# Performance work log

Hardware: AMD Instinct MI355X
Metric: run time of the kernel (lower is better)

## Reference

```python
import jax, jax.numpy as jnp
import numpy as np

N = 200_000        # atoms
E = 800_000        # directed edges (pairs e, e^1 are mutual reverses)
H = 512            # hidden_size
AF = 133           # atom_feat_size
BF = 14            # bond_feat_size
B = 4096           # num graphs


def setup_inputs() -> dict:
    key = jax.random.key(0)
    ks = jax.random.split(key, 8)
    atom_hiddens = jax.random.normal(ks[0], (N, H), dtype=jnp.float32)
    # undirected bonds, then interleave as (src,dst),(dst,src) so rev[e] = e ^ 1
    src = jax.random.randint(ks[1], (E // 2,), 0, N, dtype=jnp.int32)
    dst = jax.random.randint(ks[2], (E // 2,), 0, N, dtype=jnp.int32)
    heads = jnp.stack([src, dst], axis=1).reshape(-1)   # [E]
    tails = jnp.stack([dst, src], axis=1).reshape(-1)   # [E]
    edge_index = jnp.stack([heads, tails], axis=0)      # [2, E]
    rev_edge_index = jnp.arange(E, dtype=jnp.int32) ^ 1
    batch = jnp.sort(jax.random.randint(ks[3], (N,), 0, B, dtype=jnp.int32))
    batch = batch.at[-1].set(B - 1)  # batch[-1]+1 == B, matching the torch code
    s = 1.0 / np.sqrt(H)
    return {
        "atom_hiddens": atom_hiddens,
        "W_node": jax.random.normal(ks[4], (H, AF), dtype=jnp.float32) * s,
        "b_node": jnp.zeros((AF,), dtype=jnp.float32),
        "W_edge": jax.random.normal(ks[5], (H, BF), dtype=jnp.float32) * s,
        "b_edge": jnp.zeros((BF,), dtype=jnp.float32),
        "W_g1": jax.random.normal(ks[6], (H, H), dtype=jnp.float32) * s,
        "b_g1": jnp.zeros((H,), dtype=jnp.float32),
        "W_g2": jax.random.normal(ks[7], (H, 1), dtype=jnp.float32) * s,
        "b_g2": jnp.zeros((1,), dtype=jnp.float32),
        "edge_index": edge_index,
        "rev_edge_index": rev_edge_index,
        "batch": batch,
        "num_graphs": B,
    }


def reference(atom_hiddens, W_node, b_node, W_edge, b_edge, W_g1, b_g1,
              W_g2, b_g2, edge_index, rev_edge_index, batch, num_graphs):
    # graph pooling: index_add_ over the sorted batch vector
    graph_emb = jax.ops.segment_sum(atom_hiddens, batch, num_segments=num_graphs)
    # node head
    node_pred = atom_hiddens @ W_node + b_node
    # edge dedup: the torch loop keeps edge e iff its reverse was not yet
    # visited, i.e. iff e < rev_edge_index[e] (rev is an involution), giving
    # exactly E//2 kept edges.
    e_ids = jnp.arange(edge_index.shape[1])
    keep = jnp.nonzero(e_ids < rev_edge_index, size=edge_index.shape[1] // 2,
                       fill_value=0)[0]
    a1 = edge_index[0, keep]
    a2 = edge_index[1, keep]
    bond_emb = 0.5 * (atom_hiddens[a1] + atom_hiddens[a2])  # [E//2, H]
    edge_pred = bond_emb @ W_edge + b_edge
    # graph head: Linear -> ReLU -> Linear
    graph_pred = jax.nn.relu(graph_emb @ W_g1 + b_g1) @ W_g2 + b_g2
    return node_pred, edge_pred, graph_pred
```

## Files before the change

kernel.cpp:

```cpp
#include <hip/hip_runtime.h>

#define NATOMS 200000
#define NEDGE  800000
#define NBOND  400000
#define HDIM   512
#define AF     133
#define BFEAT  14
#define NGRAPH 4096

#define NODE_OUT_SZ (NATOMS * AF)
#define EDGE_OUT_SZ (NBOND * BFEAT)

#define WS_P     0
#define WS_BMAT  12800000
#define WS_BIAS  12963840
#define WS_GEF   12964480
#define WS_WG1T  21353088

typedef _Float16 half8 __attribute__((ext_vector_type(8)));
typedef float floatx4 __attribute__((ext_vector_type(4)));

__global__ void pack_kernel(const float* __restrict__ Wn, const float* __restrict__ bn,
                            const float* __restrict__ We, const float* __restrict__ be,
                            const float* __restrict__ Wg1, const float* __restrict__ bg2,
                            _Float16* __restrict__ Bmat, float* __restrict__ bias,
                            _Float16* __restrict__ Wg1t, float* __restrict__ gpred) {
    int idx = blockIdx.x * 256 + threadIdx.x;
    if (idx < 160 * 512) {
        int n = idx >> 9, k = idx & 511;
        float v = 0.f;
        if (n < AF)              v = Wn[k * AF + n];
        else if (n < AF + BFEAT) v = We[k * BFEAT + (n - AF)];
        Bmat[idx] = (_Float16)v;
    } else if (idx < 160 * 512 + 512 * 512) {
        int i = idx - 160 * 512;
        int n = i >> 9, k = i & 511;
        Wg1t[i] = (_Float16)Wg1[k * HDIM + n];
    } else if (idx < 160 * 512 + 512 * 512 + 160) {
        int n = idx - (160 * 512 + 512 * 512);
        float v = 0.f;
        if (n < AF)              v = bn[n];
        else if (n < AF + BFEAT) v = be[n - AF];
        bias[n] = v;
    } else if (idx < 160 * 512 + 512 * 512 + 160 + NGRAPH) {
        gpred[idx - (160 * 512 + 512 * 512 + 160)] = bg2[0];
    }
}

__global__ void zero_ge(float4* __restrict__ GEf4) {
    GEf4[blockIdx.x * 256 + threadIdx.x] = make_float4(0.f, 0.f, 0.f, 0.f);
}

__global__ __launch_bounds__(256) void gemm_node(const float* __restrict__ A,
                                                 const _Float16* __restrict__ Bm,
                                                 const float* __restrict__ bias,
                                                 const int* __restrict__ batch,
                                                 float* __restrict__ node_out,
                                                 float* __restrict__ P,
                                                 float* __restrict__ GEf) {
    __shared__ _Float16 As[128][72];
    __shared__ _Float16 Bs[160][72];
    __shared__ int bg[128];

    const int t    = threadIdx.x;
    const int bm   = blockIdx.x;
    const int w    = t >> 6, l = t & 63, quad = l >> 4, lr = l & 15;
    const int wm   = w & 1, wn = w >> 1;

    if (t < 128) {
        int grow = bm * 128 + t;
        bg[t] = (grow < NATOMS) ? batch[grow] : -1;
    }

    floatx4 acc[4][5];
    for (int mt = 0; mt < 4; ++mt)
        for (int nt = 0; nt < 5; ++nt)
            acc[mt][nt] = (floatx4){0.f, 0.f, 0.f, 0.f};

    const int arow0 = t >> 2;
    const int aseg  = (t & 3) * 16;
    const int pc    = t & 63;
    const int pq    = w;

    for (int ko = 0; ko < 8; ++ko) {
        const int k0 = ko * 64;
        float4 av[2][4];
        for (int p = 0; p < 2; ++p) {
            int row = arow0 + p * 64;
            long grow = (long)bm * 128 + row;
            if (grow < NATOMS) {
                const float4* src = (const float4*)(A + grow * HDIM + k0 + aseg);
                av[p][0] = src[0]; av[p][1] = src[1]; av[p][2] = src[2]; av[p][3] = src[3];
            } else {
                av[p][0] = av[p][1] = av[p][2] = av[p][3] = make_float4(0.f, 0.f, 0.f, 0.f);
            }
        }
        uint4 bv[5];
        for (int it = 0; it < 5; ++it) {
            int idx = t + it * 256;
            int row = idx >> 3, c = (idx & 7) * 8;
            bv[it] = *(const uint4*)(Bm + row * HDIM + k0 + c);
        }
        __syncthreads();
        for (int p = 0; p < 2; ++p) {
            int row = arow0 + p * 64;
            half8 h0 = {(_Float16)av[p][0].x, (_Float16)av[p][0].y, (_Float16)av[p][0].z, (_Float16)av[p][0].w,
                        (_Float16)av[p][1].x, (_Float16)av[p][1].y, (_Float16)av[p][1].z, (_Float16)av[p][1].w};
            half8 h1 = {(_Float16)av[p][2].x, (_Float16)av[p][2].y, (_Float16)av[p][2].z, (_Float16)av[p][2].w,
                        (_Float16)av[p][3].x, (_Float16)av[p][3].y, (_Float16)av[p][3].z, (_Float16)av[p][3].w};
            *(half8*)&As[row][aseg]     = h0;
            *(half8*)&As[row][aseg + 8] = h1;
        }
        for (int it = 0; it < 5; ++it) {
            int idx = t + it * 256;
            int row = idx >> 3, c = (idx & 7) * 8;
            *(uint4*)&Bs[row][c] = bv[it];
        }
        __syncthreads();
        for (int kk = 0; kk < 64; kk += 32) {
            half8 af[4], bf[5];
            for (int mt = 0; mt < 4; ++mt)
                af[mt] = *(const half8*)&As[wm * 64 + mt * 16 + lr][kk + quad * 8];
            for (int nt = 0; nt < 5; ++nt)
                bf[nt] = *(const half8*)&Bs[wn * 80 + nt * 16 + lr][kk + quad * 8];
            for (int mt = 0; mt < 4; ++mt)
                for (int nt = 0; nt < 5; ++nt)
                    acc[mt][nt] = __builtin_amdgcn_mfma_f32_16x16x32_f16(af[mt], bf[nt], acc[mt][nt], 0, 0, 0);
        }
        {
            float psum = 0.f;
            int pg = bg[pq * 32];
            for (int r = pq * 32; r < pq * 32 + 32; ++r) {
                int gid = bg[r];
                if (gid != pg) {
                    if (pg >= 0) atomicAdd(&GEf[(size_t)pg * HDIM + k0 + pc], psum);
                    psum = 0.f; pg = gid;
                }
                psum += (float)As[r][pc];
            }
            if (pg >= 0) atomicAdd(&GEf[(size_t)pg * HDIM + k0 + pc], psum);
        }
    }

    float biasv[5];
    for (int nt = 0; nt < 5; ++nt) biasv[nt] = bias[wn * 80 + nt * 16 + lr];
    for (int mt = 0; mt < 4; ++mt) {
        int rbase = bm * 128 + wm * 64 + mt * 16 + quad * 4;
        for (int r = 0; r < 4; ++r) {
            int grow = rbase + r;
            if (grow >= NATOMS) continue;
            for (int nt = 0; nt < 5; ++nt) {
                int gcol = wn * 80 + nt * 16 + lr;
                float v = acc[mt][nt][r] + biasv[nt];
                if (gcol < AF)                  node_out[(long)grow * AF + gcol] = v;
                else if (gcol < AF + BFEAT)     P[(long)grow * 16 + (gcol - AF)] = v;
            }
        }
    }
}

__global__ __launch_bounds__(256) void edge_kernel(const int* __restrict__ ei,
                                                   const float* __restrict__ P,
                                                   float* __restrict__ eout) {
    int t  = threadIdx.x;
    int j  = t & 15, bi = t >> 4;
    int b  = blockIdx.x * 16 + bi;
    if (b >= NBOND) return;
    if (j < BFEAT) {
        int e  = 2 * b;
        int a1 = ei[e];
        int a2 = ei[NEDGE + e];
        float v = 0.5f * (P[(size_t)a1 * 16 + j] + P[(size_t)a2 * 16 + j]);
        eout[(size_t)b * BFEAT + j] = v;
    }
}

__global__ __launch_bounds__(256) void gemm_graph(const float* __restrict__ GEf,
                                                  const _Float16* __restrict__ Bt,
                                                  const float* __restrict__ bg1,
                                                  const float* __restrict__ wg2,
                                                  float* __restrict__ gpred) {
    __shared__ _Float16 As[128][72];
    __shared__ _Float16 Bs[128][72];

    const int t   = threadIdx.x;
    const int bmb = blockIdx.x, bnb = blockIdx.y;
    const int w   = t >> 6, l = t & 63, quad = l >> 4, lr = l & 15;
    const int wm  = w & 1, wn = w >> 1;

    floatx4 acc[4][4];
    for (int mt = 0; mt < 4; ++mt)
        for (int nt = 0; nt < 4; ++nt)
            acc[mt][nt] = (floatx4){0.f, 0.f, 0.f, 0.f};

    const int arow0 = t >> 2;
    const int aseg  = (t & 3) * 16;

    for (int ko = 0; ko < 8; ++ko) {
        const int k0 = ko * 64;
        float4 av[2][4];
        for (int p = 0; p < 2; ++p) {
            int row = bmb * 128 + arow0 + p * 64;
            const float4* src = (const float4*)(GEf + (size_t)row * HDIM + k0 + aseg);
            av[p][0] = src[0]; av[p][1] = src[1]; av[p][2] = src[2]; av[p][3] = src[3];
        }
        uint4 bvv[4];
        for (int it = 0; it < 4; ++it) {
            int idx = t + it * 256;
            int row = idx >> 3, c = (idx & 7) * 8;
            bvv[it] = *(const uint4*)(Bt + (size_t)(bnb * 128 + row) * HDIM + k0 + c);
        }
        __syncthreads();
        for (int p = 0; p < 2; ++p) {
            int row = arow0 + p * 64;
            half8 h0 = {(_Float16)av[p][0].x, (_Float16)av[p][0].y, (_Float16)av[p][0].z, (_Float16)av[p][0].w,
                        (_Float16)av[p][1].x, (_Float16)av[p][1].y, (_Float16)av[p][1].z, (_Float16)av[p][1].w};
            half8 h1 = {(_Float16)av[p][2].x, (_Float16)av[p][2].y, (_Float16)av[p][2].z, (_Float16)av[p][2].w,
                        (_Float16)av[p][3].x, (_Float16)av[p][3].y, (_Float16)av[p][3].z, (_Float16)av[p][3].w};
            *(half8*)&As[row][aseg]     = h0;
            *(half8*)&As[row][aseg + 8] = h1;
        }
        for (int it = 0; it < 4; ++it) {
            int idx = t + it * 256;
            int row = idx >> 3, c = (idx & 7) * 8;
            *(uint4*)&Bs[row][c] = bvv[it];
        }
        __syncthreads();
        for (int kk = 0; kk < 64; kk += 32) {
            half8 af[4], bf[4];
            for (int mt = 0; mt < 4; ++mt)
                af[mt] = *(const half8*)&As[wm * 64 + mt * 16 + lr][kk + quad * 8];
            for (int nt = 0; nt < 4; ++nt)
                bf[nt] = *(const half8*)&Bs[wn * 64 + nt * 16 + lr][kk + quad * 8];
            for (int mt = 0; mt < 4; ++mt)
                for (int nt = 0; nt < 4; ++nt)
                    acc[mt][nt] = __builtin_amdgcn_mfma_f32_16x16x32_f16(af[mt], bf[nt], acc[mt][nt], 0, 0, 0);
        }
    }

    float bg1v[4], wg2v[4];
    for (int nt = 0; nt < 4; ++nt) {
        int col = bnb * 128 + wn * 64 + nt * 16 + lr;
        bg1v[nt] = bg1[col];
        wg2v[nt] = wg2[col];
    }
    for (int mt = 0; mt < 4; ++mt) {
        for (int r = 0; r < 4; ++r) {
            int row = bmb * 128 + wm * 64 + mt * 16 + quad * 4 + r;
            float partial = 0.f;
            for (int nt = 0; nt < 4; ++nt) {
                float v = acc[mt][nt][r] + bg1v[nt];
                v = v > 0.f ? v : 0.f;
                partial += v * wg2v[nt];
            }
            partial += __shfl_xor(partial, 1);
            partial += __shfl_xor(partial, 2);
            partial += __shfl_xor(partial, 4);
            partial += __shfl_xor(partial, 8);
            if (lr == 0) atomicAdd(&gpred[row], partial);
        }
    }
}

extern "C" void kernel_launch(void* const* d_in, const int* in_sizes, int n_in,
                              void* d_out, int out_size, void* d_ws, size_t ws_size,
                              hipStream_t stream) {
    const float* A    = (const float*)d_in[0];
    const float* Wn   = (const float*)d_in[1];
    const float* bn   = (const float*)d_in[2];
    const float* We   = (const float*)d_in[3];
    const float* be   = (const float*)d_in[4];
    const float* Wg1  = (const float*)d_in[5];
    const float* bg1  = (const float*)d_in[6];
    const float* Wg2  = (const float*)d_in[7];
    const float* bg2  = (const float*)d_in[8];
    const int*   ei   = (const int*)d_in[9];
    const int*   batch= (const int*)d_in[11];

    char* ws = (char*)d_ws;
    float*    P    = (float*)(ws + WS_P);
    _Float16* Bmat = (_Float16*)(ws + WS_BMAT);
    float*    bias = (float*)(ws + WS_BIAS);
    float*    GEf  = (float*)(ws + WS_GEF);
    _Float16* Wg1t = (_Float16*)(ws + WS_WG1T);

    float* node_out = (float*)d_out;
    float* edge_out = node_out + NODE_OUT_SZ;
    float* gpred    = edge_out + EDGE_OUT_SZ;

    pack_kernel<<<dim3(1361), dim3(256), 0, stream>>>(Wn, bn, We, be, Wg1, bg2, Bmat, bias, Wg1t, gpred);
    zero_ge<<<dim3(NGRAPH * HDIM / 4 / 256), dim3(256), 0, stream>>>((float4*)GEf);
    gemm_node<<<dim3((NATOMS + 127) / 128), dim3(256), 0, stream>>>(A, Bmat, bias, batch, node_out, P, GEf);
    edge_kernel<<<dim3(NBOND / 16), dim3(256), 0, stream>>>(ei, P, edge_out);
    gemm_graph<<<dim3(32, 4), dim3(256), 0, stream>>>(GEf, Wg1t, bg1, Wg2, gpred);
}
```

Baseline: 747.0 us.

## Prefetch next K tile in node GEMM, vectorize edge kernel, tile weight packing

The node GEMM now issues the global loads for the next 64-wide K slice before running the MFMA work on the current slice, and writes them to shared memory after compute. This hides global memory latency behind the matrix math. The edge kernel switches to float4 loads, with 4 threads per bond instead of 16, to reduce load instructions. The pack kernel uses shared-memory tiled transposes for coalesced weight transposition, and unroll pragmas are added throughout. The prefetch adds an extra barrier per iteration and raises register pressure, which could lower occupancy.

```diff
diff --git a/kernel.cpp b/kernel.cpp
--- a/kernel.cpp
+++ b/kernel.cpp
@@ -20,30 +20,47 @@
 typedef _Float16 half8 __attribute__((ext_vector_type(8)));
 typedef float floatx4 __attribute__((ext_vector_type(4)));
 
-__global__ void pack_kernel(const float* __restrict__ Wn, const float* __restrict__ bn,
-                            const float* __restrict__ We, const float* __restrict__ be,
-                            const float* __restrict__ Wg1, const float* __restrict__ bg2,
-                            _Float16* __restrict__ Bmat, float* __restrict__ bias,
-                            _Float16* __restrict__ Wg1t, float* __restrict__ gpred) {
-    int idx = blockIdx.x * 256 + threadIdx.x;
-    if (idx < 160 * 512) {
-        int n = idx >> 9, k = idx & 511;
-        float v = 0.f;
-        if (n < AF)              v = Wn[k * AF + n];
-        else if (n < AF + BFEAT) v = We[k * BFEAT + (n - AF)];
-        Bmat[idx] = (_Float16)v;
-    } else if (idx < 160 * 512 + 512 * 512) {
-        int i = idx - 160 * 512;
-        int n = i >> 9, k = i & 511;
-        Wg1t[i] = (_Float16)Wg1[k * HDIM + n];
-    } else if (idx < 160 * 512 + 512 * 512 + 160) {
-        int n = idx - (160 * 512 + 512 * 512);
-        float v = 0.f;
-        if (n < AF)              v = bn[n];
-        else if (n < AF + BFEAT) v = be[n - AF];
-        bias[n] = v;
-    } else if (idx < 160 * 512 + 512 * 512 + 160 + NGRAPH) {
-        gpred[idx - (160 * 512 + 512 * 512 + 160)] = bg2[0];
+__global__ __launch_bounds__(256) void pack_kernel(
+        const float* __restrict__ Wn, const float* __restrict__ bn,
+        const float* __restrict__ We, const float* __restrict__ be,
+        const float* __restrict__ Wg1, const float* __restrict__ bg2,
+        _Float16* __restrict__ Bmat, float* __restrict__ bias,
+        _Float16* __restrict__ Wg1t, float* __restrict__ gpred) {
+    __shared__ float tile[64][65];
+    const int b = blockIdx.x, t = threadIdx.x;
+    const int c = t & 63, r0 = t >> 6;
+
+    if (b < 64) {
+        int bi = b & 7, bj = b >> 3;
+        for (int r = r0; r < 64; r += 4)
+            tile[r][c] = Wg1[(size_t)(bj * 64 + r) * HDIM + bi * 64 + c];
+        __syncthreads();
+        for (int r = r0; r < 64; r += 4)
+            Wg1t[(size_t)(bi * 64 + r) * HDIM + bj * 64 + c] = (_Float16)tile[c][r];
+    } else if (b < 88) {
+        int bb = b - 64;
+        int bi = bb % 3, bj = bb / 3;
+        for (int r = r0; r < 64; r += 4) {
+            int k = bj * 64 + r, n = bi * 64 + c;
+            float v = 0.f;
+            if (n < AF)              v = Wn[(size_t)k * AF + n];
+            else if (n < AF + BFEAT) v = We[(size_t)k * BFEAT + (n - AF)];
+            tile[r][c] = v;
+        }
+        __syncthreads();
+        for (int r = r0; r < 64; r += 4) {
+            int n = bi * 64 + r;
+            if (n < 160) Bmat[(size_t)n * HDIM + bj * 64 + c] = (_Float16)tile[c][r];
+        }
+    } else {
+        for (int i = t; i < 160; i += 256) {
+            float v = 0.f;
+            if (i < AF)              v = bn[i];
+            else                     v = be[i - AF];
+            bias[i] = v;
+        }
+        float g = bg2[0];
+        for (int i = t; i < NGRAPH; i += 256) gpred[i] = g;
     }
 }
 
@@ -73,7 +90,9 @@
     }
 
     floatx4 acc[4][5];
+#pragma unroll
     for (int mt = 0; mt < 4; ++mt)
+#pragma unroll
         for (int nt = 0; nt < 5; ++nt)
             acc[mt][nt] = (floatx4){0.f, 0.f, 0.f, 0.f};
 
@@ -82,48 +101,78 @@
     const int pc    = t & 63;
     const int pq    = w;
 
+    float4 av[2][4];
+    uint4  bv[5];
+
+#pragma unroll
+    for (int p = 0; p < 2; ++p) {
+        long grow = (long)bm * 128 + arow0 + p * 64;
+        if (grow < NATOMS) {
+            const float4* src = (const float4*)(A + grow * HDIM + aseg);
+            av[p][0] = src[0]; av[p][1] = src[1]; av[p][2] = src[2]; av[p][3] = src[3];
+        } else {
+            av[p][0] = av[p][1] = av[p][2] = av[p][3] = make_float4(0.f, 0.f, 0.f, 0.f);
+        }
+    }
+#pragma unroll
+    for (int it = 0; it < 5; ++it) {
+        int idx = t + it * 256;
+        int row = idx >> 3, c = (idx & 7) * 8;
+        bv[it] = *(const uint4*)(Bm + row * HDIM + c);
+    }
+#pragma unroll
+    for (int p = 0; p < 2; ++p) {
+        int row = arow0 + p * 64;
+        half8 h0 = {(_Float16)av[p][0].x, (_Float16)av[p][0].y, (_Float16)av[p][0].z, (_Float16)av[p][0].w,
+                    (_Float16)av[p][1].x, (_Float16)av[p][1].y, (_Float16)av[p][1].z, (_Float16)av[p][1].w};
+        half8 h1 = {(_Float16)av[p][2].x, (_Float16)av[p][2].y, (_Float16)av[p][2].z, (_Float16)av[p][2].w,
+                    (_Float16)av[p][3].x, (_Float16)av[p][3].y, (_Float16)av[p][3].z, (_Float16)av[p][3].w};
+        *(half8*)&As[row][aseg]     = h0;
+        *(half8*)&As[row][aseg + 8] = h1;
+    }
+
     for (int ko = 0; ko < 8; ++ko) {
         const int k0 = ko * 64;
-        float4 av[2][4];
-        for (int p = 0; p < 2; ++p) {
-            int row = arow0 + p * 64;
-            long grow = (long)bm * 128 + row;
-            if (grow < NATOMS) {
-                const float4* src = (const float4*)(A + grow * HDIM + k0 + aseg);
-                av[p][0] = src[0]; av[p][1] = src[1]; av[p][2] = src[2]; av[p][3] = src[3];
-            } else {
-                av[p][0] = av[p][1] = av[p][2] = av[p][3] = make_float4(0.f, 0.f, 0.f, 0.f);
-            }
-        }
-        uint4 bv[5];
-        for (int it = 0; it < 5; ++it) {
-            int idx = t + it * 256;
-            int row = idx >> 3, c = (idx & 7) * 8;
-            bv[it] = *(const uint4*)(Bm + row * HDIM + k0 + c);
-        }
-        __syncthreads();
-        for (int p = 0; p < 2; ++p) {
-            int row = arow0 + p * 64;
-            half8 h0 = {(_Float16)av[p][0].x, (_Float16)av[p][0].y, (_Float16)av[p][0].z, (_Float16)av[p][0].w,
-                        (_Float16)av[p][1].x, (_Float16)av[p][1].y, (_Float16)av[p][1].z, (_Float16)av[p][1].w};
-            half8 h1 = {(_Float16)av[p][2].x, (_Float16)av[p][2].y, (_Float16)av[p][2].z, (_Float16)av[p][2].w,
-                        (_Float16)av[p][3].x, (_Float16)av[p][3].y, (_Float16)av[p][3].z, (_Float16)av[p][3].w};
-            *(half8*)&As[row][aseg]     = h0;
-            *(half8*)&As[row][aseg + 8] = h1;
-        }
+
+        __syncthreads();
+#pragma unroll
         for (int it = 0; it < 5; ++it) {
             int idx = t + it * 256;
             int row = idx >> 3, c = (idx & 7) * 8;
             *(uint4*)&Bs[row][c] = bv[it];
         }
-        __syncthreads();
+        if (ko < 7) {
+            const int k1 = k0 + 64;
+#pragma unroll
+            for (int p = 0; p < 2; ++p) {
+                long grow = (long)bm * 128 + arow0 + p * 64;
+                if (grow < NATOMS) {
+                    const float4* src = (const float4*)(A + grow * HDIM + k1 + aseg);
+                    av[p][0] = src[0]; av[p][1] = src[1]; av[p][2] = src[2]; av[p][3] = src[3];
+                } else {
+                    av[p][0] = av[p][1] = av[p][2] = av[p][3] = make_float4(0.f, 0.f, 0.f, 0.f);
+                }
+            }
+#pragma unroll
+            for (int it = 0; it < 5; ++it) {
+                int idx = t + it * 256;
+                int row = idx >> 3, c = (idx & 7) * 8;
+                bv[it] = *(const uint4*)(Bm + row * HDIM + k1 + c);
+            }
+        }
+        __syncthreads();
+#pragma unroll
         for (int kk = 0; kk < 64; kk += 32) {
             half8 af[4], bf[5];
+#pragma unroll
             for (int mt = 0; mt < 4; ++mt)
                 af[mt] = *(const half8*)&As[wm * 64 + mt * 16 + lr][kk + quad * 8];
+#pragma unroll
             for (int nt = 0; nt < 5; ++nt)
                 bf[nt] = *(const half8*)&Bs[wn * 80 + nt * 16 + lr][kk + quad * 8];
+#pragma unroll
             for (int mt = 0; mt < 4; ++mt)
+#pragma unroll
                 for (int nt = 0; nt < 5; ++nt)
                     acc[mt][nt] = __builtin_amdgcn_mfma_f32_16x16x32_f16(af[mt], bf[nt], acc[mt][nt], 0, 0, 0);
         }
@@ -140,15 +189,32 @@
             }
             if (pg >= 0) atomicAdd(&GEf[(size_t)pg * HDIM + k0 + pc], psum);
         }
+        if (ko < 7) {
+            __syncthreads();
+#pragma unroll
+            for (int p = 0; p < 2; ++p) {
+                int row = arow0 + p * 64;
+                half8 h0 = {(_Float16)av[p][0].x, (_Float16)av[p][0].y, (_Float16)av[p][0].z, (_Float16)av[p][0].w,
+                            (_Float16)av[p][1].x, (_Float16)av[p][1].y, (_Float16)av[p][1].z, (_Float16)av[p][1].w};
+                half8 h1 = {(_Float16)av[p][2].x, (_Float16)av[p][2].y, (_Float16)av[p][2].z, (_Float16)av[p][2].w,
+                            (_Float16)av[p][3].x, (_Float16)av[p][3].y, (_Float16)av[p][3].z, (_Float16)av[p][3].w};
+                *(half8*)&As[row][aseg]     = h0;
+                *(half8*)&As[row][aseg + 8] = h1;
+            }
+        }
     }
 
     float biasv[5];
+#pragma unroll
     for (int nt = 0; nt < 5; ++nt) biasv[nt] = bias[wn * 80 + nt * 16 + lr];
+#pragma unroll
     for (int mt = 0; mt < 4; ++mt) {
         int rbase = bm * 128 + wm * 64 + mt * 16 + quad * 4;
+#pragma unroll
         for (int r = 0; r < 4; ++r) {
             int grow = rbase + r;
             if (grow >= NATOMS) continue;
+#pragma unroll
             for (int nt = 0; nt < 5; ++nt) {
                 int gcol = wn * 80 + nt * 16 + lr;
                 float v = acc[mt][nt][r] + biasv[nt];
@@ -163,16 +229,21 @@
                                                    const float* __restrict__ P,
                                                    float* __restrict__ eout) {
     int t  = threadIdx.x;
-    int j  = t & 15, bi = t >> 4;
-    int b  = blockIdx.x * 16 + bi;
+    int q  = t & 3, bi = t >> 2;
+    int b  = blockIdx.x * 64 + bi;
     if (b >= NBOND) return;
-    if (j < BFEAT) {
-        int e  = 2 * b;
-        int a1 = ei[e];
-        int a2 = ei[NEDGE + e];
-        float v = 0.5f * (P[(size_t)a1 * 16 + j] + P[(size_t)a2 * 16 + j]);
-        eout[(size_t)b * BFEAT + j] = v;
-    }
+    int e  = 2 * b;
+    int a1 = ei[e];
+    int a2 = ei[NEDGE + e];
+    const float4 v1 = *(const float4*)(P + (size_t)a1 * 16 + q * 4);
+    const float4 v2 = *(const float4*)(P + (size_t)a2 * 16 + q * 4);
+    float r[4] = {0.5f * (v1.x + v2.x), 0.5f * (v1.y + v2.y),
+                  0.5f * (v1.z + v2.z), 0.5f * (v1.w + v2.w)};
+    float* dst = eout + (size_t)b * BFEAT + q * 4;
+    int rem = BFEAT - q * 4;
+#pragma unroll
+    for (int i = 0; i < 4; ++i)
+        if (i < rem) dst[i] = r[i];
 }
 
 __global__ __launch_bounds__(256) void gemm_graph(const float* __restrict__ GEf,
@@ -288,9 +359,9 @@
     float* edge_out = node_out + NODE_OUT_SZ;
     float* gpred    = edge_out + EDGE_OUT_SZ;
 
-    pack_kernel<<<dim3(1361), dim3(256), 0, stream>>>(Wn, bn, We, be, Wg1, bg2, Bmat, bias, Wg1t, gpred);
+    pack_kernel<<<dim3(89), dim3(256), 0, stream>>>(Wn, bn, We, be, Wg1, bg2, Bmat, bias, Wg1t, gpred);
     zero_ge<<<dim3(NGRAPH * HDIM / 4 / 256), dim3(256), 0, stream>>>((float4*)GEf);
     gemm_node<<<dim3((NATOMS + 127) / 128), dim3(256), 0, stream>>>(A, Bmat, bias, batch, node_out, P, GEf);
-    edge_kernel<<<dim3(NBOND / 16), dim3(256), 0, stream>>>(ei, P, edge_out);
+    edge_kernel<<<dim3((NBOND + 63) / 64), dim3(256), 0, stream>>>(ei, P, edge_out);
     gemm_graph<<<dim3(32, 4), dim3(256), 0, stream>>>(GEf, Wg1t, bg1, Wg2, gpred);
 }
```

Result: no change. 740.6 us (-0.9%).
